# Performance work log

Hardware: AMD Instinct MI355X
Metric: run time of the kernel (lower is better)

Reference implementation:

```python
import jax, jax.numpy as jnp
import numpy as np

B, T, F, U, M = 4096, 16, 256, 512, 8
DELTA_T = 0.04

# ln_tau_table: tau = 1, 10^0.5, 10^1.0, ... -> ln(tau) = i * 0.5*ln(10)
LN_TAU = (jnp.arange(M, dtype=jnp.float32) * (0.5 * np.log(10.0))).astype(jnp.float32)
DECAY = jnp.exp(-DELTA_T / (LN_TAU + 1e-7))  # [M]


def setup_inputs() -> dict:
    key = jax.random.key(0)
    ks = jax.random.split(key, 9)
    s = lambda fan_in: 1.0 / np.sqrt(fan_in)
    return {
        "x": jax.random.normal(ks[0], (B, T, F), dtype=jnp.float32),
        "W_r": jax.random.normal(ks[1], (F + U, U * M), dtype=jnp.float32) * s(F + U),
        "b_r": jax.random.normal(ks[2], (U * M,), dtype=jnp.float32) * 0.01,
        "W_q": jax.random.normal(ks[3], (F + U, U), dtype=jnp.float32) * s(F + U),
        "b_q": jax.random.normal(ks[4], (U,), dtype=jnp.float32) * 0.01,
        "W_s": jax.random.normal(ks[5], (F + U, U * M), dtype=jnp.float32) * s(F + U),
        "b_s": jax.random.normal(ks[6], (U * M,), dtype=jnp.float32) * 0.01,
        "W_out": jax.random.normal(ks[7], (U, 3), dtype=jnp.float32) * s(U),
        "b_out": jax.random.normal(ks[8], (3,), dtype=jnp.float32) * 0.01,
    }


def _ctgru_forward(x, W_r, b_r, W_q, b_q, W_s, b_s, W_out, b_out):
    def step(h_hat, x_t):  # h_hat: [B,U,M], x_t: [B,F]
        h = h_hat.sum(axis=2)                              # [B,U]
        fused = jnp.concatenate([x_t, h], axis=1)          # [B,F+U]
        ln_tau_r = (fused @ W_r + b_r).reshape(-1, U, M)   # [B,U,M]
        r_ki = jax.nn.softmax(-jnp.square(ln_tau_r - LN_TAU), axis=2)
        q_in = jnp.concatenate([x_t, jnp.sum(r_ki * h_hat, axis=2)], axis=1)
        q_k = jnp.tanh(q_in @ W_q + b_q)[:, :, None]       # [B,U,1]
        ln_tau_s = (fused @ W_s + b_s).reshape(-1, U, M)
        s_ki = jax.nn.softmax(-jnp.square(ln_tau_s - LN_TAU), axis=2)
        h_next = ((1.0 - s_ki) * h_hat + s_ki * q_k) * DECAY
        return h_next, h_next.sum(axis=2)                  # carry, hidden [B,U]

    h0 = jnp.zeros((x.shape[0], U, M), dtype=x.dtype)
    _, hiddens = jax.lax.scan(step, h0, jnp.swapaxes(x, 0, 1))  # hiddens: [T,B,U]
    outputs = jnp.swapaxes(hiddens, 0, 1)                  # [B,T,U]
    return outputs @ W_out + b_out                         # [B,T,3]


def reference(x, W_r, b_r, W_q, b_q, W_s, b_s, W_out, b_out):
    return _ctgru_forward(x, W_r, b_r, W_q, b_q, W_s, b_s, W_out, b_out)
```

## Files before the change

### kernel.cpp

```cpp
#include <hip/hip_runtime.h>
#include <hip/hip_bf16.h>
#include <math.h>

#define B_   4096
#define T_   16
#define F_   256
#define U_   512
#define M_   8
#define K_   768
#define NRS  4096
#define NC   8192
#define LNT  1.1512925f

typedef __bf16 bf16_t;
typedef bf16_t bf16x8 __attribute__((ext_vector_type(8)));
typedef bf16_t bf16x4 __attribute__((ext_vector_type(4)));
typedef float  f32x4  __attribute__((ext_vector_type(4)));

__device__ inline void gl_lds16(const void* g, void* lds) {
    __builtin_amdgcn_global_load_lds(
        (const __attribute__((address_space(1))) unsigned int*)g,
        (__attribute__((address_space(3))) unsigned int*)lds, 16, 0, 0);
}

#define VMCNT(n) asm volatile("s_waitcnt vmcnt(" #n ")" ::: "memory")
#define LGKM0()  asm volatile("s_waitcnt lgkmcnt(0)" ::: "memory")
#define BAR()    __builtin_amdgcn_s_barrier()

__device__ inline void stageA(bf16_t* dst, const bf16_t* xt, const bf16_t* hp,
                              int m0, int k0, int tid) {
    const int r = tid >> 2;
    const int c = ((tid & 3) ^ ((tid >> 3) & 3)) * 8;
    const bf16_t *s0, *s1;
    if (k0 < F_) {
        s0 = xt + (size_t)(m0 + r) * F_ + k0 + c;
        s1 = xt + (size_t)(m0 + r + 128) * F_ + k0 + c;
    } else {
        s0 = hp + (size_t)(m0 + r) * U_ + (k0 - F_) + c;
        s1 = hp + (size_t)(m0 + r + 128) * U_ + (k0 - F_) + c;
    }
    gl_lds16(s0, (char*)dst + tid * 16);
    gl_lds16(s1, (char*)dst + (tid + 512) * 16);
}

__device__ inline void stageB(bf16_t* dst, const bf16_t* Bt, int n0, int k0, int tid) {
    const int r = tid >> 2;
    const int c = ((tid & 3) ^ ((tid >> 3) & 3)) * 8;
    gl_lds16(Bt + (size_t)(n0 + r) * K_ + k0 + c,       (char*)dst + tid * 16);
    gl_lds16(Bt + (size_t)(n0 + r + 128) * K_ + k0 + c, (char*)dst + (tid + 512) * 16);
}

__device__ inline void ds_read4(const bf16_t* base, bf16x8 (&v)[4]) {
    v[0] = *(const bf16x8*)(base);
    v[1] = *(const bf16x8*)(base + 512);
    v[2] = *(const bf16x8*)(base + 1024);
    v[3] = *(const bf16x8*)(base + 1536);
}

template <int H>
__device__ inline void mfma16(f32x4 (&acc)[8][4], const bf16x8 (&a)[4],
                              const bf16x8 (&b)[4]) {
    __builtin_amdgcn_s_setprio(1);
#pragma unroll
    for (int i = 0; i < 4; ++i)
#pragma unroll
        for (int j = 0; j < 4; ++j)
            acc[H * 4 + i][j] = __builtin_amdgcn_mfma_f32_16x16x32_bf16(
                a[i], b[j], acc[H * 4 + i][j], 0, 0, 0);
    __builtin_amdgcn_s_setprio(0);
}

__global__ __launch_bounds__(512, 2) void gemm_rs_8ph(
    const bf16_t* __restrict__ xt,
    const bf16_t* __restrict__ hprev,
    const bf16_t* __restrict__ Bt,
    const float*  __restrict__ biasP,
    const bf16_t* __restrict__ hhat,
    bf16_t* __restrict__ rh,
    bf16_t* __restrict__ sbuf)
{
    __shared__ bf16_t Asl[2][2][256 * 32];
    __shared__ bf16_t Bsl[2][2][256 * 32];

    const int tid  = threadIdx.x;
    const int lane = tid & 63;
    const int wave = tid >> 6;

    const int lin = blockIdx.y * 16 + blockIdx.x;
    const int xcd = lin & 7, q = lin >> 3;
    const int m0 = ((xcd >> 1) * 4 + (q & 3)) * 256;
    const int n0 = ((xcd & 1) * 16 + (q >> 2)) * 256;

    const int wm = wave >> 2;
    const int wn = wave & 3;
    const int lr = lane & 15;
    const int kq = lane >> 4;
    const int cr = (kq ^ ((lr >> 1) & 3)) * 8;

    const int aoff0 = (wm * 128 + lr) * 32 + cr;
    const int aoff1 = (wm * 128 + 64 + lr) * 32 + cr;
    const int boff  = (wn * 64 + lr) * 32 + cr;

    f32x4 acc[8][4] = {};
    bf16x8 a[4], b[4];

    stageA(&Asl[0][0][0], xt, hprev, m0, 0,  tid);
    stageB(&Bsl[0][0][0], Bt, n0, 0,  tid);
    stageA(&Asl[1][0][0], xt, hprev, m0, 32, tid);
    stageB(&Bsl[1][0][0], Bt, n0, 32, tid);
    stageA(&Asl[0][1][0], xt, hprev, m0, 64, tid);
    stageB(&Bsl[0][1][0], Bt, n0, 64, tid);
    VMCNT(8);
    BAR();

#define TILE(T, VM2, VM4, S12, S34)                                           \
  {                                                                           \
    const int p_ = (T) & 1, pn_ = p_ ^ 1;                                     \
                                   \
    ds_read4(&Asl[0][p_][0] + aoff0, a);                                      \
    ds_read4(&Bsl[0][p_][0] + boff, b);                                       \
    if (S12) stageA(&Asl[1][pn_][0], xt, hprev, m0, ((T) + 1) * 64 + 32, tid);\
    LGKM0();                                                                  \
    mfma16<0>(acc, a, b);                                                     \
                                                                     \
    ds_read4(&Asl[0][p_][0] + aoff1, a);                                      \
    if (S12) stageB(&Bsl[1][pn_][0], Bt, n0, ((T) + 1) * 64 + 32, tid);       \
    VMCNT(VM2); BAR(); LGKM0();                                               \
    mfma16<1>(acc, a, b);                                                     \
    BAR();                                                                    \
                                                        \
    ds_read4(&Asl[1][p_][0] + aoff0, a);                                      \
    ds_read4(&Bsl[1][p_][0] + boff, b);                                       \
    if (S34) stageA(&Asl[0][p_][0], xt, hprev, m0, ((T) + 2) * 64, tid);      \
    LGKM0();                                                                  \
    mfma16<0>(acc, a, b);                                                     \
                                                                     \
    ds_read4(&Asl[1][p_][0] + aoff1, a);                                      \
    if (S34) stageB(&Bsl[0][p_][0], Bt, n0, ((T) + 2) * 64, tid);             \
    VMCNT(VM4); BAR(); LGKM0();                                               \
    mfma16<1>(acc, a, b);                                                     \
    BAR();                                                                    \
  }

    for (int tt = 0; tt < 10; ++tt) TILE(tt, 8, 8, 1, 1);
    TILE(10, 8, 4, 1, 0);
    TILE(11, 0, 0, 0, 0);
#undef TILE

    const int nb  = n0 + wn * 64;
    const int u3  = lane & 7;
    const int m0v = ((lane >> 3) & 1) * 4;
    const bool is_r = nb < NRS;

    float bj[4];
#pragma unroll
    for (int j = 0; j < 4; ++j) bj[j] = biasP[nb + j * 16 + lr];

#pragma unroll
    for (int mi = 0; mi < 8; ++mi) {
        const int rowb = m0 + wm * 128 + mi * 16 + kq * 4;
#pragma unroll
        for (int r = 0; r < 4; ++r) {
            const int row = rowb + r;
            float e[4], sum = 0.f;
#pragma unroll
            for (int j = 0; j < 4; ++j) {
                float v = acc[mi][j][r] + bj[j];
                float d = v - (float)(m0v + j) * LNT;
                e[j] = __expf(-d * d);
                sum += e[j];
            }
            sum += __shfl_xor(sum, 8, 64);
            const float inv = 1.0f / sum;
            if (is_r) {
                bf16x4 h4 = *(const bf16x4*)(hhat + (size_t)row * NRS + nb + u3 * 8 + m0v);
                float rhv = 0.f;
#pragma unroll
                for (int j = 0; j < 4; ++j) rhv += e[j] * inv * (float)h4[j];
                rhv += __shfl_xor(rhv, 8, 64);
                if ((lane & 8) == 0)
                    rh[(size_t)row * U_ + (nb >> 3) + u3] = (bf16_t)rhv;
            } else {
                bf16x4 pv;
#pragma unroll
                for (int j = 0; j < 4; ++j) pv[j] = (bf16_t)(e[j] * inv);
                *(bf16x4*)(sbuf + (size_t)row * NRS + (nb - NRS) + u3 * 8 + m0v) = pv;
            }
        }
    }
}

__global__ __launch_bounds__(256) void gemm_q_up(
    const bf16_t* __restrict__ xt,
    const bf16_t* __restrict__ rh,
    const bf16_t* __restrict__ Bq,
    const float*  __restrict__ bq,
    const bf16_t* __restrict__ sbuf,
    bf16_t* __restrict__ hhat,
    bf16_t* __restrict__ hnext)
{
    __shared__ bf16_t Al[2][64 * 32];
    __shared__ bf16_t Bl[2][64 * 32];

    const int tid  = threadIdx.x;
    const int lane = tid & 63;
    const int wave = tid >> 6;
    const int m0 = blockIdx.x * 64;
    const int n0 = blockIdx.y * 64;
    const int wm = (wave & 1) * 32;
    const int wn = (wave >> 1) * 32;
    const int lr = lane & 15;
    const int kq = lane >> 4;

    f32x4 acc[2][2] = {};

    const int rA = tid >> 2;
    const int kc = (tid & 3) * 8;

    for (int kk = 0; kk < K_; kk += 64) {
        const bf16_t* arow;
        int cbase;
        if (kk < F_) { arow = xt + (size_t)(m0 + rA) * F_; cbase = kk; }
        else         { arow = rh + (size_t)(m0 + rA) * U_; cbase = kk - F_; }

        __syncthreads();
        gl_lds16(arow + cbase + kc,      (char*)&Al[0][0] + tid * 16);
        gl_lds16(arow + cbase + 32 + kc, (char*)&Al[1][0] + tid * 16);
        gl_lds16(Bq + (size_t)(n0 + rA) * K_ + kk + kc,      (char*)&Bl[0][0] + tid * 16);
        gl_lds16(Bq + (size_t)(n0 + rA) * K_ + kk + 32 + kc, (char*)&Bl[1][0] + tid * 16);
        __syncthreads();

#pragma unroll
        for (int s = 0; s < 2; s++) {
            bf16x8 af[2], bfr[2];
#pragma unroll
            for (int i = 0; i < 2; i++)
                af[i] = *(const bf16x8*)(&Al[s][0] + (wm + i * 16 + lr) * 32 + kq * 8);
#pragma unroll
            for (int i = 0; i < 2; i++)
                bfr[i] = *(const bf16x8*)(&Bl[s][0] + (wn + i * 16 + lr) * 32 + kq * 8);
#pragma unroll
            for (int i = 0; i < 2; i++)
#pragma unroll
                for (int j = 0; j < 2; j++)
                    acc[i][j] = __builtin_amdgcn_mfma_f32_16x16x32_bf16(
                        af[i], bfr[j], acc[i][j], 0, 0, 0);
        }
    }

    const float DEC[8] = {0.0f, 0.9658531f, 0.9827783f, 0.9884856f,
                          0.9913518f, 0.9930754f, 0.9942261f, 0.9950489f};

#pragma unroll
    for (int i = 0; i < 2; i++) {
        const int rowb = m0 + wm + i * 16 + kq * 4;
#pragma unroll
        for (int j = 0; j < 2; j++) {
            const int u = n0 + wn + j * 16 + lr;
            const float bv = bq[u];
#pragma unroll
            for (int r = 0; r < 4; r++) {
                const int row = rowb + r;
                const float q = tanhf(acc[i][j][r] + bv);
                const size_t base = (size_t)row * NRS + u * 8;
                bf16x8 s8 = *(const bf16x8*)(sbuf + base);
                bf16x8 h8 = *(const bf16x8*)(hhat + base);
                bf16x8 ho;
                float hs = 0.f;
#pragma unroll
                for (int m = 0; m < 8; m++) {
                    float s = (float)s8[m];
                    float h = (float)h8[m];
                    float hn = ((1.f - s) * h + s * q) * DEC[m];
                    ho[m] = (bf16_t)hn;
                    hs += hn;
                }
                *(bf16x8*)(hhat + base) = ho;
                hnext[(size_t)row * U_ + u] = (bf16_t)hs;
            }
        }
    }
}

__global__ void transpose_perm(const float* __restrict__ src, bf16_t* __restrict__ dst) {
    __shared__ float tl[32][33];
    int k0 = blockIdx.x * 32, n0 = blockIdx.y * 32;
    int tx = threadIdx.x & 31, ty = threadIdx.x >> 5;
#pragma unroll
    for (int i = 0; i < 32; i += 8)
        tl[ty + i][tx] = src[(size_t)(k0 + ty + i) * NRS + n0 + tx];
    __syncthreads();
#pragma unroll
    for (int i = 0; i < 32; i += 8) {
        int n = n0 + ty + i;
        int m = n & 7, u3v = (n >> 3) & 7;
        int p = (n & ~63) + (m & 3) * 16 + (m >> 2) * 8 + u3v;
        dst[(size_t)p * K_ + k0 + tx] = (bf16_t)tl[tx][ty + i];
    }
}

__global__ void transpose_plain(const float* __restrict__ src, bf16_t* __restrict__ dst, int N) {
    __shared__ float tl[32][33];
    int k0 = blockIdx.x * 32, n0 = blockIdx.y * 32;
    int tx = threadIdx.x & 31, ty = threadIdx.x >> 5;
#pragma unroll
    for (int i = 0; i < 32; i += 8)
        tl[ty + i][tx] = src[(size_t)(k0 + ty + i) * N + n0 + tx];
    __syncthreads();
#pragma unroll
    for (int i = 0; i < 32; i += 8)
        dst[(size_t)(n0 + ty + i) * K_ + k0 + tx] = (bf16_t)tl[tx][ty + i];
}

__global__ void bias_perm(const float* __restrict__ b_r, const float* __restrict__ b_s,
                          float* __restrict__ biasP) {
    int p = blockIdx.x * 256 + threadIdx.x;
    int pr = p & 63, j = pr >> 4, lr = pr & 15;
    int L = (p & ~63) + (lr & 7) * 8 + ((lr >> 3) & 1) * 4 + j;
    biasP[p] = (L < NRS) ? b_r[L] : b_s[L - NRS];
}

__global__ void xall_build(const float* __restrict__ x, bf16_t* __restrict__ xall) {
    int idx = blockIdx.x * 256 + threadIdx.x;
    int b = idx >> 12;
    int rem = idx & 4095;
    int t = rem >> 8, f = rem & 255;
    xall[((size_t)t * B_ + b) * F_ + f] = (bf16_t)x[idx];
}

__global__ __launch_bounds__(256) void out_all(
    const bf16_t* __restrict__ hall,
    const float* __restrict__ Wout,
    const float* __restrict__ bout,
    float* __restrict__ out)
{
    int row = blockIdx.x * 4 + (threadIdx.x >> 6);
    int lane = threadIdx.x & 63;
    bf16x8 h8 = *(const bf16x8*)(hall + (size_t)row * U_ + lane * 8);
    float p0 = 0, p1 = 0, p2 = 0;
#pragma unroll
    for (int k = 0; k < 8; k++) {
        float h = (float)h8[k];
        int u = lane * 8 + k;
        p0 += h * Wout[u * 3 + 0];
        p1 += h * Wout[u * 3 + 1];
        p2 += h * Wout[u * 3 + 2];
    }
    for (int off = 32; off; off >>= 1) {
        p0 += __shfl_down(p0, off, 64);
        p1 += __shfl_down(p1, off, 64);
        p2 += __shfl_down(p2, off, 64);
    }
    if (lane == 0) {
        int t = row >> 12, b = row & (B_ - 1);
        size_t o = ((size_t)b * T_ + t) * 3;
        out[o + 0] = p0 + bout[0];
        out[o + 1] = p1 + bout[1];
        out[o + 2] = p2 + bout[2];
    }
}

extern "C" void kernel_launch(void* const* d_in, const int* in_sizes, int n_in,
                              void* d_out, int out_size, void* d_ws, size_t ws_size,
                              hipStream_t stream) {
    const float* x   = (const float*)d_in[0];
    const float* W_r = (const float*)d_in[1];
    const float* b_r = (const float*)d_in[2];
    const float* W_q = (const float*)d_in[3];
    const float* b_q = (const float*)d_in[4];
    const float* W_s = (const float*)d_in[5];
    const float* b_s = (const float*)d_in[6];
    const float* W_o = (const float*)d_in[7];
    const float* b_o = (const float*)d_in[8];
    float* out = (float*)d_out;

    char* ws = (char*)d_ws;
    bf16_t* hhat  = (bf16_t*)ws; ws += (size_t)B_ * NRS * 2;
    bf16_t* sbuf  = (bf16_t*)ws; ws += (size_t)B_ * NRS * 2;
    bf16_t* xall  = (bf16_t*)ws; ws += (size_t)B_ * T_ * F_ * 2;
    bf16_t* hall  = (bf16_t*)ws; ws += (size_t)(T_ + 1) * B_ * U_ * 2;
    bf16_t* rh    = (bf16_t*)ws; ws += (size_t)B_ * U_ * 2;
    bf16_t* WrsT  = (bf16_t*)ws; ws += (size_t)NC * K_ * 2;
    bf16_t* WqT   = (bf16_t*)ws; ws += (size_t)U_ * K_ * 2;
    float*  biasP = (float*)ws;  ws += (size_t)NC * 4;

    hipMemsetAsync(hhat, 0, (size_t)B_ * NRS * 2, stream);
    hipMemsetAsync(hall, 0, (size_t)B_ * U_ * 2, stream);
    xall_build<<<B_ * T_ * F_ / 256, 256, 0, stream>>>(x, xall);
    transpose_perm<<<dim3(K_ / 32, NRS / 32), 256, 0, stream>>>(W_r, WrsT);
    transpose_perm<<<dim3(K_ / 32, NRS / 32), 256, 0, stream>>>(W_s, WrsT + (size_t)NRS * K_);
    transpose_plain<<<dim3(K_ / 32, U_ / 32), 256, 0, stream>>>(W_q, WqT, U_);
    bias_perm<<<NC / 256, 256, 0, stream>>>(b_r, b_s, biasP);

    for (int t = 0; t < T_; t++) {
        const bf16_t* xt = xall + (size_t)t * B_ * F_;
        const bf16_t* hp = hall + (size_t)t * B_ * U_;
        bf16_t*       hn = hall + (size_t)(t + 1) * B_ * U_;
        gemm_rs_8ph<<<dim3(16, 32), 512, 0, stream>>>(xt, hp, WrsT, biasP, hhat, rh, sbuf);
        gemm_q_up<<<dim3(64, 8), 256, 0, stream>>>(xt, rh, WqT, b_q, sbuf, hhat, hn);
    }
    out_all<<<B_ * T_ / 4, 256, 0, stream>>>(hall + (size_t)B_ * U_, W_o, b_o, out);
}
```

Baseline: 1.727 ms.

## Replace eight-phase LDS pipeline with simple two-stage double buffering

The RS GEMM kernel drops its four-slot, 64-wide k-pipeline with partial vmcnt waits in favour of a two-buffer scheme over 32-wide k-steps. Each step issues the next stage's global-to-LDS loads, runs both MFMA halves, then waits for all loads and syncs. This halves shared memory use and simplifies the schedule. The cost is a full memory drain and barrier every step, which exposes load latency.

```diff
diff --git a/kernel.cpp b/kernel.cpp
--- a/kernel.cpp
+++ b/kernel.cpp
@@ -70,7 +70,7 @@
     __builtin_amdgcn_s_setprio(0);
 }
 
-__global__ __launch_bounds__(512, 2) void gemm_rs_8ph(
+__global__ __launch_bounds__(512, 2) void gemm_rs_p2(
     const bf16_t* __restrict__ xt,
     const bf16_t* __restrict__ hprev,
     const bf16_t* __restrict__ Bt,
@@ -79,8 +79,8 @@
     bf16_t* __restrict__ rh,
     bf16_t* __restrict__ sbuf)
 {
-    __shared__ bf16_t Asl[2][2][256 * 32];
-    __shared__ bf16_t Bsl[2][2][256 * 32];
+    __shared__ bf16_t Asl[2][256 * 32];
+    __shared__ bf16_t Bsl[2][256 * 32];
 
     const int tid  = threadIdx.x;
     const int lane = tid & 63;
@@ -104,47 +104,32 @@
     f32x4 acc[8][4] = {};
     bf16x8 a[4], b[4];
 
-    stageA(&Asl[0][0][0], xt, hprev, m0, 0,  tid);
-    stageB(&Bsl[0][0][0], Bt, n0, 0,  tid);
-    stageA(&Asl[1][0][0], xt, hprev, m0, 32, tid);
-    stageB(&Bsl[1][0][0], Bt, n0, 32, tid);
-    stageA(&Asl[0][1][0], xt, hprev, m0, 64, tid);
-    stageB(&Bsl[0][1][0], Bt, n0, 64, tid);
-    VMCNT(8);
+    stageA(&Asl[0][0], xt, hprev, m0, 0, tid);
+    stageB(&Bsl[0][0], Bt, n0, 0, tid);
+    VMCNT(0);
     BAR();
 
-#define TILE(T, VM2, VM4, S12, S34)                                           \
+#define TILE(T, SFLAG)                                                        \
   {                                                                           \
     const int p_ = (T) & 1, pn_ = p_ ^ 1;                                     \
-                                   \
-    ds_read4(&Asl[0][p_][0] + aoff0, a);                                      \
-    ds_read4(&Bsl[0][p_][0] + boff, b);                                       \
-    if (S12) stageA(&Asl[1][pn_][0], xt, hprev, m0, ((T) + 1) * 64 + 32, tid);\
+    if (SFLAG) {                                                              \
+      stageA(&Asl[pn_][0], xt, hprev, m0, ((T) + 1) * 32, tid);               \
+      stageB(&Bsl[pn_][0], Bt, n0, ((T) + 1) * 32, tid);                      \
+    }                                                                         \
+    ds_read4(&Asl[p_][0] + aoff0, a);                                         \
+    ds_read4(&Bsl[p_][0] + boff, b);                                          \
     LGKM0();                                                                  \
     mfma16<0>(acc, a, b);                                                     \
-                                                                     \
-    ds_read4(&Asl[0][p_][0] + aoff1, a);                                      \
-    if (S12) stageB(&Bsl[1][pn_][0], Bt, n0, ((T) + 1) * 64 + 32, tid);       \
-    VMCNT(VM2); BAR(); LGKM0();                                               \
+    ds_read4(&Asl[p_][0] + aoff1, a);                                         \
+    LGKM0();                                                                  \
     mfma16<1>(acc, a, b);                                                     \
-    BAR();                                                                    \
-                                                        \
-    ds_read4(&Asl[1][p_][0] + aoff0, a);                                      \
-    ds_read4(&Bsl[1][p_][0] + boff, b);                                       \
-    if (S34) stageA(&Asl[0][p_][0], xt, hprev, m0, ((T) + 2) * 64, tid);      \
-    LGKM0();                                                                  \
-    mfma16<0>(acc, a, b);                                                     \
-                                                                     \
-    ds_read4(&Asl[1][p_][0] + aoff1, a);                                      \
-    if (S34) stageB(&Bsl[0][p_][0], Bt, n0, ((T) + 2) * 64, tid);             \
-    VMCNT(VM4); BAR(); LGKM0();                                               \
-    mfma16<1>(acc, a, b);                                                     \
+    VMCNT(0);                                                                 \
     BAR();                                                                    \
   }
 
-    for (int tt = 0; tt < 10; ++tt) TILE(tt, 8, 8, 1, 1);
-    TILE(10, 8, 4, 1, 0);
-    TILE(11, 0, 0, 0, 0);
+    for (int tt = 0; tt < 22; tt += 2) { TILE(tt, 1); TILE(tt + 1, 1); }
+    TILE(22, 1);
+    TILE(23, 0);
 #undef TILE
 
     const int nb  = n0 + wn * 64;
@@ -396,7 +381,7 @@
         const bf16_t* xt = xall + (size_t)t * B_ * F_;
         const bf16_t* hp = hall + (size_t)t * B_ * U_;
         bf16_t*       hn = hall + (size_t)(t + 1) * B_ * U_;
-        gemm_rs_8ph<<<dim3(16, 32), 512, 0, stream>>>(xt, hp, WrsT, biasP, hhat, rh, sbuf);
+        gemm_rs_p2<<<dim3(16, 32), 512, 0, stream>>>(xt, hp, WrsT, biasP, hhat, rh, sbuf);
         gemm_q_up<<<dim3(64, 8), 256, 0, stream>>>(xt, rh, WqT, b_q, sbuf, hhat, hn);
     }
     out_all<<<B_ * T_ / 4, 256, 0, stream>>>(hall + (size_t)B_ * U_, W_o, b_o, out);
```

Measured after the change: 1.803 ms. 1.04x slower.
